# Kernel optimization log

Measured on AMD Instinct MI355X. Metric: run time of the kernel, lower is better.

## Reference

```python
import jax, jax.numpy as jnp
import numpy as np

INPUT_LENGTH = 4096
NUM_FEATURES = 10000
KERNEL_LENGTH = 9
NUM_KERNELS = 84
EPS = 1e-12


def _compute_dilations(input_length):
    # mirrors MiniRocketTransform._compute_dilations exactly
    max_dilation = (input_length - 1) // (KERNEL_LENGTH - 1)
    dilations = np.logspace(0, np.log10(max_dilation), num=NUM_KERNELS, base=2, dtype=int)
    return np.unique(dilations).tolist()

DILATIONS = _compute_dilations(INPUT_LENGTH)  # static python ints


def _generate_kernels(seed=42):
    # mirrors MiniRocketTransform._generate_kernels; kernels with sum==0 dropped
    rng = np.random.RandomState(seed)
    ks = []
    for _ in range(NUM_KERNELS):
        k = rng.choice([-1, 2], size=KERNEL_LENGTH, p=[2.0 / 3.0, 1.0 / 3.0])
        if k.sum() != 0:
            ks.append(k)
    return np.asarray(ks, dtype=np.float32)


def setup_inputs() -> dict:
    key = jax.random.key(0)
    x = jax.random.normal(key, (256, 1, INPUT_LENGTH), dtype=jnp.float32)
    kernels = jnp.asarray(_generate_kernels())  # (Kn, 9)
    return {"x": x, "kernels": kernels}


def reference(x, kernels):
    # x: (B, 1, L); kernels: (Kn, 9) of {-1, 2}
    B = x.shape[0]
    w = kernels[:, None, :]  # (Kn, 1, 9) OIH

    # zero-stuffed dilated kernel + padding=0 (len((1,1,K) tensor)//2 == 0)
    # is exactly a VALID conv with rhs_dilation=d.
    def conv(xv, wv, d):
        return jax.lax.conv_general_dilated(
            xv, wv, window_strides=(1,), padding='VALID', rhs_dilation=(d,))

    # biases computed ONCE from the first kernel / first dilation conv output
    conv0 = conv(x, w[:1], DILATIONS[0])  # (B, 1, L0)
    q = jnp.quantile(conv0, jnp.array([0.25, 0.5, 0.75], dtype=conv0.dtype), axis=2)  # (3, B, 1)
    biases = q.mean(axis=1).reshape(3)  # (3,)

    feats = []
    for d in DILATIONS:  # small static set (~6)
        c = conv(x, w, d)  # (B, Kn, Ld)
        # PPV: fraction of positions where conv output exceeds each bias
        ppv = (c[:, :, None, :] > biases[None, None, :, None]).astype(jnp.float32).mean(axis=3)  # (B, Kn, 3)
        feats.append(ppv)

    # feature order in torch: kernel-major, then dilation, then bias
    f = jnp.stack(feats, axis=2).reshape(B, -1)  # (B, Kn*Dn*3)
    out = jnp.zeros((B, NUM_FEATURES), dtype=jnp.float32).at[:, :f.shape[1]].set(f)
    # F.normalize(p=2, dim=-1, eps=1e-12)
    norm = jnp.maximum(jnp.linalg.norm(out, axis=-1, keepdims=True), EPS)
    return out / norm
```

## Files before the change

### kernel.cpp

```cpp
#include <hip/hip_runtime.h>
#include <stdint.h>

#define IN_LEN 4096
#define NFEAT  10000

__device__ __forceinline__ void count_gt_f32(unsigned& cnt, float thr, float val) {
  asm volatile("v_cmp_lt_f32 vcc, %1, %2\n\t"
               "v_addc_co_u32 %0, vcc, 0, %0, vcc"
               : "+v"(cnt)
               : "v"(thr), "v"(val)
               : "vcc");
}
__device__ __forceinline__ void count_le_u32(unsigned& cnt, unsigned mid, unsigned key) {
  asm volatile("v_cmp_ge_u32 vcc, %1, %2\n\t"
               "v_addc_co_u32 %0, vcc, 0, %0, vcc"
               : "+v"(cnt)
               : "v"(mid), "v"(key)
               : "vcc");
}

__device__ __forceinline__ unsigned key_of(float f) {
  unsigned u = __float_as_uint(f);
  return (u & 0x80000000u) ? ~u : (u | 0x80000000u);
}
__device__ __forceinline__ float key_inv(unsigned k) {
  unsigned u = (k & 0x80000000u) ? (k ^ 0x80000000u) : ~k;
  return __uint_as_float(u);
}

__global__ __launch_bounds__(256) void quant_kernel(const float* __restrict__ x,
                                                    const float* __restrict__ kern,
                                                    float* __restrict__ ws_q) {
  const int b = blockIdx.x, tid = threadIdx.x;
  __shared__ __align__(16) float xs[IN_LEN];
  __shared__ unsigned redc[2][3 * 4];

  const float4* xg = (const float4*)(x + (size_t)b * IN_LEN);
  float4* xs4 = (float4*)xs;
  for (int i = tid; i < IN_LEN / 4; i += 256) xs4[i] = xg[i];

  float w[9];
#pragma unroll
  for (int j = 0; j < 9; j++) w[j] = kern[j];
  __syncthreads();

  const int L = IN_LEN - 8;
  unsigned keys[16];
#pragma unroll
  for (int i = 0; i < 16; i++) {
    int t = tid + (i << 8);
    if (t < L) {
      float c = 0.f;
#pragma unroll
      for (int j = 0; j < 9; j++) c = fmaf(w[j], xs[t + j], c);
      keys[i] = key_of(c);
    } else {
      keys[i] = 0xFFFFFFFFu;
    }
  }

  const int targ[6] = {1021, 1022, 2043, 2044, 3065, 3066};
  unsigned lo[6], hi[6];
#pragma unroll
  for (int q = 0; q < 6; q++) { lo[q] = 0u; hi[q] = 0xFFFFFFFFu; }

  const int wave = tid >> 6, lane = tid & 63;
  for (int it = 0; it < 32; ++it) {
    const int buf = it & 1;
    unsigned mid[6], cnt[6];
#pragma unroll
    for (int q = 0; q < 6; q++) { mid[q] = lo[q] + ((hi[q] - lo[q]) >> 1); cnt[q] = 0u; }
#pragma unroll
    for (int i = 0; i < 16; i++)
#pragma unroll
      for (int q = 0; q < 6; q++) count_le_u32(cnt[q], mid[q], keys[i]);
    unsigned r[3];
#pragma unroll
    for (int q = 0; q < 3; q++) r[q] = cnt[2 * q] | (cnt[2 * q + 1] << 16);
#pragma unroll
    for (int q = 0; q < 3; q++) {
#pragma unroll
      for (int off = 32; off > 0; off >>= 1) r[q] += (unsigned)__shfl_xor((int)r[q], off);
    }
    if (lane == 0) {
#pragma unroll
      for (int q = 0; q < 3; q++) redc[buf][q * 4 + wave] = r[q];
    }
    __syncthreads();
#pragma unroll
    for (int q = 0; q < 3; q++) {
      unsigned tot = redc[buf][q * 4 + 0] + redc[buf][q * 4 + 1] +
                     redc[buf][q * 4 + 2] + redc[buf][q * 4 + 3];
      unsigned t0 = tot & 0xFFFFu, t1 = tot >> 16;
      if (t0 >= (unsigned)(targ[2 * q] + 1)) hi[2 * q] = mid[2 * q]; else lo[2 * q] = mid[2 * q] + 1;
      if (t1 >= (unsigned)(targ[2 * q + 1] + 1)) hi[2 * q + 1] = mid[2 * q + 1]; else lo[2 * q + 1] = mid[2 * q + 1] + 1;
    }
  }

  if (tid == 0) {
    float v[6];
#pragma unroll
    for (int q = 0; q < 6; q++) v[q] = key_inv(lo[q]);
    ws_q[b * 3 + 0] = v[0] + 0.75f * (v[1] - v[0]);
    ws_q[b * 3 + 1] = v[2] + 0.5f  * (v[3] - v[2]);
    ws_q[b * 3 + 2] = v[4] + 0.25f * (v[5] - v[4]);
  }
}

__global__ __launch_bounds__(256) void bias_kernel(const float* __restrict__ ws_q,
                                                   float* __restrict__ ws_bias, int B) {
  __shared__ float red[256];
  const int tid = threadIdx.x;
  for (int q = 0; q < 3; q++) {
    float v = 0.f;
    for (int i = tid; i < B; i += 256) v += ws_q[i * 3 + q];
    red[tid] = v;
    __syncthreads();
    for (int s = 128; s > 0; s >>= 1) {
      if (tid < s) red[tid] += red[tid + s];
      __syncthreads();
    }
    if (tid == 0) ws_bias[q] = red[0] / (float)B;
    __syncthreads();
  }
}

template <int D>
__device__ __forceinline__ void run_feat(const float* xs,
                                         const float* __restrict__ kern,
                                         float b0, float b1, float b2,
                                         float* __restrict__ out, int K, int b) {
  const int tid = threadIdx.x;
  const int wave = tid >> 6, lane = tid & 63;
  constexpr int L = IN_LEN - 8 * D;
  constexpr int NFULL = 31;
  constexpr int KT = 8;

  const int KPW = (K + 3) >> 2;
  const int kstart = wave * KPW;
  const int kend = (kstart + KPW < K) ? (kstart + KPW) : K;

  for (int k0 = kstart; k0 < kend; k0 += KT) {
    float w[KT][9];
#pragma unroll
    for (int kk = 0; kk < KT; kk++) {
      const int kidx = (k0 + kk < K) ? (k0 + kk) : (K - 1);
      const bool ok = (k0 + kk) < kend;
      const float* wp = kern + (size_t)kidx * 9;
#pragma unroll
      for (int j = 0; j < 9; j++) w[kk][j] = ok ? wp[j] : 0.f;
    }
    unsigned c0[KT], c1[KT], c2[KT];
#pragma unroll
    for (int kk = 0; kk < KT; kk++) { c0[kk] = 0u; c1[kk] = 0u; c2[kk] = 0u; }

#pragma unroll 1
    for (int p = 0; p < NFULL; ++p) {
      const int t = (p << 7) + lane;
      float tax[9], tay[9];
#pragma unroll
      for (int j = 0; j < 9; j++) {
        tax[j] = xs[t + j * D];
        tay[j] = xs[t + 64 + j * D];
      }
#pragma unroll
      for (int kk = 0; kk < KT; kk++) {
        float ca = 0.f, cb = 0.f;
#pragma unroll
        for (int j = 0; j < 9; j++) {
          ca = fmaf(w[kk][j], tax[j], ca);
          cb = fmaf(w[kk][j], tay[j], cb);
        }
        count_gt_f32(c0[kk], b0, ca); count_gt_f32(c0[kk], b0, cb);
        count_gt_f32(c1[kk], b1, ca); count_gt_f32(c1[kk], b1, cb);
        count_gt_f32(c2[kk], b2, ca); count_gt_f32(c2[kk], b2, cb);
      }
    }
    {
      const int t = (NFULL << 7) + lane;
      const bool v0 = t < L, v1 = (t + 64) < L;
      float tax[9], tay[9];
#pragma unroll
      for (int j = 0; j < 9; j++) {
        tax[j] = xs[t + j * D];
        tay[j] = xs[t + 64 + j * D];
      }
#pragma unroll
      for (int kk = 0; kk < KT; kk++) {
        float ca = 0.f, cb = 0.f;
#pragma unroll
        for (int j = 0; j < 9; j++) {
          ca = fmaf(w[kk][j], tax[j], ca);
          cb = fmaf(w[kk][j], tay[j], cb);
        }
        ca = v0 ? ca : -3.0e38f;
        cb = v1 ? cb : -3.0e38f;
        count_gt_f32(c0[kk], b0, ca); count_gt_f32(c0[kk], b0, cb);
        count_gt_f32(c1[kk], b1, ca); count_gt_f32(c1[kk], b1, cb);
        count_gt_f32(c2[kk], b2, ca); count_gt_f32(c2[kk], b2, cb);
      }
    }

#pragma unroll
    for (int kk = 0; kk < KT; kk++) {
      unsigned r0 = c0[kk] | (c2[kk] << 16);
      unsigned r1 = c1[kk];
#pragma unroll
      for (int off = 32; off > 0; off >>= 1) {
        r0 += (unsigned)__shfl_xor((int)r0, off);
        r1 += (unsigned)__shfl_xor((int)r1, off);
      }
      const int k = k0 + kk;
      if (lane == 0 && k < kend) {
        float* o = out + (size_t)b * NFEAT + (size_t)k * 18 + (D - 1) * 3;
        o[0] = (float)(r0 & 0xFFFFu) / (float)L;
        o[1] = (float)r1 / (float)L;
        o[2] = (float)(r0 >> 16) / (float)L;
      }
    }
  }
}

__global__ __launch_bounds__(256) void feat_kernel(const float* __restrict__ x,
                                                   const float* __restrict__ kern,
                                                   const float* __restrict__ ws_bias,
                                                   float* __restrict__ out, int K) {
  __shared__ __align__(16) float xs[IN_LEN + 48];
  const int b = blockIdx.y, tid = threadIdx.x;

  const float4* xg = (const float4*)(x + (size_t)b * IN_LEN);
  float4* xs4 = (float4*)xs;
  for (int i = tid; i < IN_LEN / 4; i += 256) xs4[i] = xg[i];
  if (tid < 48) xs[IN_LEN + tid] = 0.f;
  const float b0 = ws_bias[0], b1 = ws_bias[1], b2 = ws_bias[2];
  __syncthreads();

  switch (blockIdx.x) {
    case 0: run_feat<1>(xs, kern, b0, b1, b2, out, K, b); break;
    case 1: run_feat<2>(xs, kern, b0, b1, b2, out, K, b); break;
    case 2: run_feat<3>(xs, kern, b0, b1, b2, out, K, b); break;
    case 3: run_feat<4>(xs, kern, b0, b1, b2, out, K, b); break;
    case 4: run_feat<5>(xs, kern, b0, b1, b2, out, K, b); break;
    case 5: run_feat<6>(xs, kern, b0, b1, b2, out, K, b); break;
  }
}

__global__ __launch_bounds__(256) void norm_kernel(float* __restrict__ out, int F) {
  const int b = blockIdx.x, tid = threadIdx.x;
  __shared__ float red[256];
  float acc = 0.f;
  for (int i = tid; i < F; i += 256) {
    float v = out[(size_t)b * NFEAT + i];
    acc = fmaf(v, v, acc);
  }
  red[tid] = acc;
  __syncthreads();
  for (int s = 128; s > 0; s >>= 1) {
    if (tid < s) red[tid] += red[tid + s];
    __syncthreads();
  }
  const float inv = 1.0f / fmaxf(sqrtf(red[0]), 1e-12f);
  for (int i = tid; i < F; i += 256) out[(size_t)b * NFEAT + i] *= inv;
}

extern "C" void kernel_launch(void* const* d_in, const int* in_sizes, int n_in,
                              void* d_out, int out_size, void* d_ws, size_t ws_size,
                              hipStream_t stream) {
  const float* x = (const float*)d_in[0];
  const float* kern = (const float*)d_in[1];
  float* out = (float*)d_out;
  const int B = in_sizes[0] / IN_LEN;
  const int K = in_sizes[1] / 9;

  float* ws_q = (float*)d_ws;
  float* ws_bias = ws_q + B * 3;

  hipMemsetAsync(d_out, 0, (size_t)out_size * sizeof(float), stream);

  quant_kernel<<<B, 256, 0, stream>>>(x, kern, ws_q);
  bias_kernel<<<1, 256, 0, stream>>>(ws_q, ws_bias, B);
  dim3 g(6, B);
  feat_kernel<<<g, 256, 0, stream>>>(x, kern, ws_bias, out, K);
  norm_kernel<<<B, 256, 0, stream>>>(out, K * 18);
}
```

Baseline: 231.2 us.

## Split feature convolution along sequence into halves with atomic count accumulation

Splits each (dilation, batch) block into two halves of the time axis via a third grid dimension, so twice as many blocks run with half the shared-memory footprint, and merges partial PPV counts with integer atomics into a workspace buffer. The normalization kernel now converts the counts to fractions, writes the full output row including the zero padding, and replaces the separate memset of the output. It also shrinks the kernel tile from 8 to 4, raises launch bounds for occupancy, and rewrites the compare-count asm to use SGPR condition masks with a scalar threshold instead of VCC. The costs are extra atomics, a small memset of the count buffer, and some redundant halo loads.

```diff
diff --git a/kernel.cpp b/kernel.cpp
--- a/kernel.cpp
+++ b/kernel.cpp
@@ -2,21 +2,24 @@
 #include <stdint.h>
 
 #define IN_LEN 4096
+#define HLEN   2048
 #define NFEAT  10000
 
-__device__ __forceinline__ void count_gt_f32(unsigned& cnt, float thr, float val) {
-  asm volatile("v_cmp_lt_f32 vcc, %1, %2\n\t"
-               "v_addc_co_u32 %0, vcc, 0, %0, vcc"
-               : "+v"(cnt)
-               : "v"(thr), "v"(val)
-               : "vcc");
-}
-__device__ __forceinline__ void count_le_u32(unsigned& cnt, unsigned mid, unsigned key) {
-  asm volatile("v_cmp_ge_u32 vcc, %1, %2\n\t"
-               "v_addc_co_u32 %0, vcc, 0, %0, vcc"
-               : "+v"(cnt)
-               : "v"(mid), "v"(key)
-               : "vcc");
+__device__ __forceinline__ void count2_gt_f32(unsigned& cnt, unsigned long long& cc,
+                                              float thr, float a, float b) {
+  asm("v_cmp_lt_f32 %[cc], %[t], %[va]\n\t"
+      "v_addc_co_u32 %[c], %[cc], 0, %[c], %[cc]\n\t"
+      "v_cmp_lt_f32 %[cc], %[t], %[vb]\n\t"
+      "v_addc_co_u32 %[c], %[cc], 0, %[c], %[cc]"
+      : [c] "+v"(cnt), [cc] "=&s"(cc)
+      : [t] "s"(thr), [va] "v"(a), [vb] "v"(b));
+}
+__device__ __forceinline__ void count_le_u32(unsigned& cnt, unsigned long long& cc,
+                                             unsigned mid, unsigned key) {
+  asm("v_cmp_ge_u32 %[cc], %[m], %[k]\n\t"
+      "v_addc_co_u32 %[c], %[cc], 0, %[c], %[cc]"
+      : [c] "+v"(cnt), [cc] "=&s"(cc)
+      : [m] "s"(mid), [k] "v"(key));
 }
 
 __device__ __forceinline__ unsigned key_of(float f) {
@@ -68,12 +71,13 @@
   for (int it = 0; it < 32; ++it) {
     const int buf = it & 1;
     unsigned mid[6], cnt[6];
+    unsigned long long ccq[3];
 #pragma unroll
     for (int q = 0; q < 6; q++) { mid[q] = lo[q] + ((hi[q] - lo[q]) >> 1); cnt[q] = 0u; }
 #pragma unroll
     for (int i = 0; i < 16; i++)
 #pragma unroll
-      for (int q = 0; q < 6; q++) count_le_u32(cnt[q], mid[q], keys[i]);
+      for (int q = 0; q < 6; q++) count_le_u32(cnt[q], ccq[q >> 1], mid[q], keys[i]);
     unsigned r[3];
 #pragma unroll
     for (int q = 0; q < 3; q++) r[q] = cnt[2 * q] | (cnt[2 * q + 1] << 16);
@@ -129,12 +133,15 @@
 __device__ __forceinline__ void run_feat(const float* xs,
                                          const float* __restrict__ kern,
                                          float b0, float b1, float b2,
-                                         float* __restrict__ out, int K, int b) {
+                                         unsigned* __restrict__ cnt_row, int K, int zofs) {
   const int tid = threadIdx.x;
   const int wave = tid >> 6, lane = tid & 63;
   constexpr int L = IN_LEN - 8 * D;
-  constexpr int NFULL = 31;
-  constexpr int KT = 8;
+  constexpr int KT = 4;
+
+  const int NV = zofs ? (L - HLEN) : HLEN;
+  const int FP = NV >> 7;
+  const bool hasTail = (NV & 127) != 0;
 
   const int KPW = (K + 3) >> 2;
   const int kstart = wave * KPW;
@@ -153,9 +160,10 @@
     unsigned c0[KT], c1[KT], c2[KT];
 #pragma unroll
     for (int kk = 0; kk < KT; kk++) { c0[kk] = 0u; c1[kk] = 0u; c2[kk] = 0u; }
+    unsigned long long ccA, ccB, ccC;
 
 #pragma unroll 1
-    for (int p = 0; p < NFULL; ++p) {
+    for (int p = 0; p < FP; ++p) {
       const int t = (p << 7) + lane;
       float tax[9], tay[9];
 #pragma unroll
@@ -171,14 +179,14 @@
           ca = fmaf(w[kk][j], tax[j], ca);
           cb = fmaf(w[kk][j], tay[j], cb);
         }
-        count_gt_f32(c0[kk], b0, ca); count_gt_f32(c0[kk], b0, cb);
-        count_gt_f32(c1[kk], b1, ca); count_gt_f32(c1[kk], b1, cb);
-        count_gt_f32(c2[kk], b2, ca); count_gt_f32(c2[kk], b2, cb);
-      }
-    }
-    {
-      const int t = (NFULL << 7) + lane;
-      const bool v0 = t < L, v1 = (t + 64) < L;
+        count2_gt_f32(c0[kk], ccA, b0, ca, cb);
+        count2_gt_f32(c1[kk], ccB, b1, ca, cb);
+        count2_gt_f32(c2[kk], ccC, b2, ca, cb);
+      }
+    }
+    if (hasTail) {
+      const int t = (FP << 7) + lane;
+      const bool v0 = t < NV, v1 = (t + 64) < NV;
       float tax[9], tay[9];
 #pragma unroll
       for (int j = 0; j < 9; j++) {
@@ -195,9 +203,9 @@
         }
         ca = v0 ? ca : -3.0e38f;
         cb = v1 ? cb : -3.0e38f;
-        count_gt_f32(c0[kk], b0, ca); count_gt_f32(c0[kk], b0, cb);
-        count_gt_f32(c1[kk], b1, ca); count_gt_f32(c1[kk], b1, cb);
-        count_gt_f32(c2[kk], b2, ca); count_gt_f32(c2[kk], b2, cb);
+        count2_gt_f32(c0[kk], ccA, b0, ca, cb);
+        count2_gt_f32(c1[kk], ccB, b1, ca, cb);
+        count2_gt_f32(c2[kk], ccC, b2, ca, cb);
       }
     }
 
@@ -212,45 +220,59 @@
       }
       const int k = k0 + kk;
       if (lane == 0 && k < kend) {
-        float* o = out + (size_t)b * NFEAT + (size_t)k * 18 + (D - 1) * 3;
-        o[0] = (float)(r0 & 0xFFFFu) / (float)L;
-        o[1] = (float)r1 / (float)L;
-        o[2] = (float)(r0 >> 16) / (float)L;
-      }
-    }
-  }
-}
-
-__global__ __launch_bounds__(256) void feat_kernel(const float* __restrict__ x,
-                                                   const float* __restrict__ kern,
-                                                   const float* __restrict__ ws_bias,
-                                                   float* __restrict__ out, int K) {
-  __shared__ __align__(16) float xs[IN_LEN + 48];
+        unsigned* o = cnt_row + (size_t)k * 18 + (D - 1) * 3;
+        atomicAdd(&o[0], r0 & 0xFFFFu);
+        atomicAdd(&o[1], r1);
+        atomicAdd(&o[2], r0 >> 16);
+      }
+    }
+  }
+}
+
+__global__ __launch_bounds__(256, 8) void feat_kernel(const float* __restrict__ x,
+                                                      const float* __restrict__ kern,
+                                                      const float* __restrict__ ws_bias,
+                                                      unsigned* __restrict__ cnt, int K) {
+  __shared__ __align__(16) float xs[HLEN + 48];
   const int b = blockIdx.y, tid = threadIdx.x;
-
-  const float4* xg = (const float4*)(x + (size_t)b * IN_LEN);
+  const int z = blockIdx.z, zofs = z * HLEN;
+
+  const float4* xg4 = (const float4*)(x + (size_t)b * IN_LEN);
   float4* xs4 = (float4*)xs;
-  for (int i = tid; i < IN_LEN / 4; i += 256) xs4[i] = xg[i];
-  if (tid < 48) xs[IN_LEN + tid] = 0.f;
+  const int z4 = z * (HLEN / 4);
+  for (int i = tid; i < (HLEN + 48) / 4; i += 256) {
+    float4 v;
+    if (z4 + i < IN_LEN / 4) v = xg4[z4 + i];
+    else { v.x = 0.f; v.y = 0.f; v.z = 0.f; v.w = 0.f; }
+    xs4[i] = v;
+  }
   const float b0 = ws_bias[0], b1 = ws_bias[1], b2 = ws_bias[2];
   __syncthreads();
 
+  unsigned* cnt_row = cnt + (size_t)b * K * 18;
   switch (blockIdx.x) {
-    case 0: run_feat<1>(xs, kern, b0, b1, b2, out, K, b); break;
-    case 1: run_feat<2>(xs, kern, b0, b1, b2, out, K, b); break;
-    case 2: run_feat<3>(xs, kern, b0, b1, b2, out, K, b); break;
-    case 3: run_feat<4>(xs, kern, b0, b1, b2, out, K, b); break;
-    case 4: run_feat<5>(xs, kern, b0, b1, b2, out, K, b); break;
-    case 5: run_feat<6>(xs, kern, b0, b1, b2, out, K, b); break;
-  }
-}
-
-__global__ __launch_bounds__(256) void norm_kernel(float* __restrict__ out, int F) {
+    case 0: run_feat<1>(xs, kern, b0, b1, b2, cnt_row, K, zofs); break;
+    case 1: run_feat<2>(xs, kern, b0, b1, b2, cnt_row, K, zofs); break;
+    case 2: run_feat<3>(xs, kern, b0, b1, b2, cnt_row, K, zofs); break;
+    case 3: run_feat<4>(xs, kern, b0, b1, b2, cnt_row, K, zofs); break;
+    case 4: run_feat<5>(xs, kern, b0, b1, b2, cnt_row, K, zofs); break;
+    case 5: run_feat<6>(xs, kern, b0, b1, b2, cnt_row, K, zofs); break;
+  }
+}
+
+__global__ __launch_bounds__(256) void norm_kernel(const unsigned* __restrict__ cnt,
+                                                   float* __restrict__ out, int K) {
   const int b = blockIdx.x, tid = threadIdx.x;
+  const int F = K * 18;
   __shared__ float red[256];
+  const unsigned* crow = cnt + (size_t)b * F;
+  float* row = out + (size_t)b * NFEAT;
+
   float acc = 0.f;
   for (int i = tid; i < F; i += 256) {
-    float v = out[(size_t)b * NFEAT + i];
+    const int di = (i % 18) / 3;
+    const float inv = 1.0f / (float)(IN_LEN - 8 * (di + 1));
+    const float v = (float)crow[i] * inv;
     acc = fmaf(v, v, acc);
   }
   red[tid] = acc;
@@ -259,8 +281,16 @@
     if (tid < s) red[tid] += red[tid + s];
     __syncthreads();
   }
-  const float inv = 1.0f / fmaxf(sqrtf(red[0]), 1e-12f);
-  for (int i = tid; i < F; i += 256) out[(size_t)b * NFEAT + i] *= inv;
+  const float inv_n = 1.0f / fmaxf(sqrtf(red[0]), 1e-12f);
+  for (int i = tid; i < NFEAT; i += 256) {
+    float v = 0.f;
+    if (i < F) {
+      const int di = (i % 18) / 3;
+      const float inv = 1.0f / (float)(IN_LEN - 8 * (di + 1));
+      v = (float)crow[i] * inv * inv_n;
+    }
+    row[i] = v;
+  }
 }
 
 extern "C" void kernel_launch(void* const* d_in, const int* in_sizes, int n_in,
@@ -272,14 +302,14 @@
   const int B = in_sizes[0] / IN_LEN;
   const int K = in_sizes[1] / 9;
 
-  float* ws_q = (float*)d_ws;
+  unsigned* cnt = (unsigned*)d_ws;
+  float* ws_q = (float*)d_ws + (size_t)B * 1536;
   float* ws_bias = ws_q + B * 3;
 
-  hipMemsetAsync(d_out, 0, (size_t)out_size * sizeof(float), stream);
-
+  hipMemsetAsync(cnt, 0, (size_t)B * K * 18 * sizeof(unsigned), stream);
   quant_kernel<<<B, 256, 0, stream>>>(x, kern, ws_q);
   bias_kernel<<<1, 256, 0, stream>>>(ws_q, ws_bias, B);
-  dim3 g(6, B);
-  feat_kernel<<<g, 256, 0, stream>>>(x, kern, ws_bias, out, K);
-  norm_kernel<<<B, 256, 0, stream>>>(out, K * 18);
-}
+  dim3 g(6, B, 2);
+  feat_kernel<<<g, 256, 0, stream>>>(x, kern, ws_bias, cnt, K);
+  norm_kernel<<<B, 256, 0, stream>>>(cnt, out, K);
+}
```

Result: no change. 235.4 us (+1.8%).

## Fuse bias reduction into quantile kernel and fold output zeroing into normalization

Applied to the files above, without the earlier changes.

The separate bias kernel is removed. The last quantile block, detected with an atomic counter in workspace, now computes the mean biases. The full-output memset is replaced by a small workspace memset, and the norm kernel writes zeros to the padding columns itself. The binary-search compare now uses scalar mid values with an SGPR condition mask instead of VCC, which may ease the dependency chain. This saves a launch and a large memset, at the cost of an atomic and a fence in the quantile kernel.

```diff
diff --git a/kernel.cpp b/kernel.cpp
--- a/kernel.cpp
+++ b/kernel.cpp
@@ -3,6 +3,10 @@
 
 #define IN_LEN 4096
 #define NFEAT  10000
+
+#define WS_CNTA 0
+#define WS_Q    2048
+#define WS_BIAS 8192
 
 __device__ __forceinline__ void count_gt_f32(unsigned& cnt, float thr, float val) {
   asm volatile("v_cmp_lt_f32 vcc, %1, %2\n\t"
@@ -11,12 +15,12 @@
                : "v"(thr), "v"(val)
                : "vcc");
 }
-__device__ __forceinline__ void count_le_u32(unsigned& cnt, unsigned mid, unsigned key) {
-  asm volatile("v_cmp_ge_u32 vcc, %1, %2\n\t"
-               "v_addc_co_u32 %0, vcc, 0, %0, vcc"
-               : "+v"(cnt)
-               : "v"(mid), "v"(key)
-               : "vcc");
+__device__ __forceinline__ void count_le_u32(unsigned& cnt, unsigned long long& cc,
+                                             unsigned mid, unsigned key) {
+  asm("v_cmp_ge_u32 %[cc], %[m], %[k]\n\t"
+      "v_addc_co_u32 %[c], %[cc], 0, %[c], %[cc]"
+      : [c] "+v"(cnt), [cc] "=&s"(cc)
+      : [m] "s"(mid), [k] "v"(key));
 }
 
 __device__ __forceinline__ unsigned key_of(float f) {
@@ -28,12 +32,18 @@
   return __uint_as_float(u);
 }
 
-__global__ __launch_bounds__(256) void quant_kernel(const float* __restrict__ x,
-                                                    const float* __restrict__ kern,
-                                                    float* __restrict__ ws_q) {
+__global__ __launch_bounds__(256) void quantbias_kernel(const float* __restrict__ x,
+                                                        const float* __restrict__ kern,
+                                                        unsigned char* __restrict__ ws) {
   const int b = blockIdx.x, tid = threadIdx.x;
+  float* ws_q = (float*)(ws + WS_Q);
+  float* ws_bias = (float*)(ws + WS_BIAS);
+  unsigned* cntA = (unsigned*)(ws + WS_CNTA);
+
   __shared__ __align__(16) float xs[IN_LEN];
   __shared__ unsigned redc[2][3 * 4];
+  __shared__ float redm[256];
+  __shared__ unsigned lastflag;
 
   const float4* xg = (const float4*)(x + (size_t)b * IN_LEN);
   float4* xs4 = (float4*)xs;
@@ -68,12 +78,13 @@
   for (int it = 0; it < 32; ++it) {
     const int buf = it & 1;
     unsigned mid[6], cnt[6];
+    unsigned long long ccq[3];
 #pragma unroll
     for (int q = 0; q < 6; q++) { mid[q] = lo[q] + ((hi[q] - lo[q]) >> 1); cnt[q] = 0u; }
 #pragma unroll
     for (int i = 0; i < 16; i++)
 #pragma unroll
-      for (int q = 0; q < 6; q++) count_le_u32(cnt[q], mid[q], keys[i]);
+      for (int q = 0; q < 6; q++) count_le_u32(cnt[q], ccq[q >> 1], mid[q], keys[i]);
     unsigned r[3];
 #pragma unroll
     for (int q = 0; q < 3; q++) r[q] = cnt[2 * q] | (cnt[2 * q + 1] << 16);
@@ -105,22 +116,27 @@
     ws_q[b * 3 + 1] = v[2] + 0.5f  * (v[3] - v[2]);
     ws_q[b * 3 + 2] = v[4] + 0.25f * (v[5] - v[4]);
   }
-}
-
-__global__ __launch_bounds__(256) void bias_kernel(const float* __restrict__ ws_q,
-                                                   float* __restrict__ ws_bias, int B) {
-  __shared__ float red[256];
-  const int tid = threadIdx.x;
+
+  __syncthreads();
+  if (tid == 0) {
+    __threadfence();
+    unsigned old = __hip_atomic_fetch_add(cntA, 1u, __ATOMIC_ACQ_REL, __HIP_MEMORY_SCOPE_AGENT);
+    lastflag = (old == gridDim.x - 1) ? 1u : 0u;
+  }
+  __syncthreads();
+  if (lastflag == 0u) return;
+  __threadfence();
+  const int B = gridDim.x;
   for (int q = 0; q < 3; q++) {
     float v = 0.f;
     for (int i = tid; i < B; i += 256) v += ws_q[i * 3 + q];
-    red[tid] = v;
+    redm[tid] = v;
     __syncthreads();
     for (int s = 128; s > 0; s >>= 1) {
-      if (tid < s) red[tid] += red[tid + s];
+      if (tid < s) redm[tid] += redm[tid + s];
       __syncthreads();
     }
-    if (tid == 0) ws_bias[q] = red[0] / (float)B;
+    if (tid == 0) ws_bias[q] = redm[0] / (float)B;
     __syncthreads();
   }
 }
@@ -223,10 +239,11 @@
 
 __global__ __launch_bounds__(256) void feat_kernel(const float* __restrict__ x,
                                                    const float* __restrict__ kern,
-                                                   const float* __restrict__ ws_bias,
+                                                   const unsigned char* __restrict__ ws,
                                                    float* __restrict__ out, int K) {
   __shared__ __align__(16) float xs[IN_LEN + 48];
   const int b = blockIdx.y, tid = threadIdx.x;
+  const float* ws_bias = (const float*)(ws + WS_BIAS);
 
   const float4* xg = (const float4*)(x + (size_t)b * IN_LEN);
   float4* xs4 = (float4*)xs;
@@ -248,9 +265,10 @@
 __global__ __launch_bounds__(256) void norm_kernel(float* __restrict__ out, int F) {
   const int b = blockIdx.x, tid = threadIdx.x;
   __shared__ float red[256];
+  float* row = out + (size_t)b * NFEAT;
   float acc = 0.f;
   for (int i = tid; i < F; i += 256) {
-    float v = out[(size_t)b * NFEAT + i];
+    float v = row[i];
     acc = fmaf(v, v, acc);
   }
   red[tid] = acc;
@@ -260,7 +278,10 @@
     __syncthreads();
   }
   const float inv = 1.0f / fmaxf(sqrtf(red[0]), 1e-12f);
-  for (int i = tid; i < F; i += 256) out[(size_t)b * NFEAT + i] *= inv;
+  for (int i = tid; i < NFEAT; i += 256) {
+    float v = (i < F) ? row[i] * inv : 0.f;
+    row[i] = v;
+  }
 }
 
 extern "C" void kernel_launch(void* const* d_in, const int* in_sizes, int n_in,
@@ -271,15 +292,11 @@
   float* out = (float*)d_out;
   const int B = in_sizes[0] / IN_LEN;
   const int K = in_sizes[1] / 9;
-
-  float* ws_q = (float*)d_ws;
-  float* ws_bias = ws_q + B * 3;
-
-  hipMemsetAsync(d_out, 0, (size_t)out_size * sizeof(float), stream);
-
-  quant_kernel<<<B, 256, 0, stream>>>(x, kern, ws_q);
-  bias_kernel<<<1, 256, 0, stream>>>(ws_q, ws_bias, B);
+  unsigned char* ws = (unsigned char*)d_ws;
+
+  hipMemsetAsync(ws, 0, 2048, stream);
+  quantbias_kernel<<<B, 256, 0, stream>>>(x, kern, ws);
   dim3 g(6, B);
-  feat_kernel<<<g, 256, 0, stream>>>(x, kern, ws_bias, out, K);
+  feat_kernel<<<g, 256, 0, stream>>>(x, kern, ws, out, K);
   norm_kernel<<<B, 256, 0, stream>>>(out, K * 18);
 }
```

Result: slower. 240.0 us (+3.8%).
